# Kernel tuning notes

Hardware: AMD Instinct MI355X
Metric: run time of the kernel (lower is better)

## Reference

```python
import jax, jax.numpy as jnp
import numpy as np

B, S, HID = 4, 1024, 768
H, D = 12, 32              # attention_head_size = (HID/H)//2
AH = H * D                 # all_head_size = 384
SCALING = D ** (-0.5)


def setup_inputs() -> dict:
    key = jax.random.key(0)
    ks = jax.random.split(key, 6)
    hidden_states = jax.random.normal(ks[0], (B, S, HID), dtype=jnp.float32)
    attention_mask = jnp.zeros((B, 1, 1, S), dtype=jnp.float32)
    init = 0.02
    Wq = jax.random.normal(ks[1], (AH, HID), dtype=jnp.float32) * init
    Wk1 = jax.random.normal(ks[2], (AH, HID), dtype=jnp.float32) * init
    Wk2 = jax.random.normal(ks[3], (AH, HID), dtype=jnp.float32) * init
    Wv = jax.random.normal(ks[4], (AH, HID), dtype=jnp.float32) * init
    bq = jnp.zeros((AH,), jnp.float32)
    bk1 = jnp.zeros((AH,), jnp.float32)
    bk2 = jnp.zeros((AH,), jnp.float32)
    bv = jnp.zeros((AH,), jnp.float32)
    pi = jnp.ones((2, H), jnp.float32) / 2.0
    return {"hidden_states": hidden_states, "attention_mask": attention_mask,
            "Wq": Wq, "bq": bq, "Wk1": Wk1, "bk1": bk1, "Wk2": Wk2, "bk2": bk2,
            "Wv": Wv, "bv": bv, "pi": pi}


def _heads(x):
    # [B,S,AH] -> [B,H,S,D]
    return x.reshape(B, S, H, D).transpose(0, 2, 1, 3)


def _sq_dist(x1, x2):
    # gpytorch Distance._sq_dist (postprocess=False): mean-adjust, then
    # ||x1||^2 + ||x2||^2 - 2 x1 x2^T, clamped at 0.
    adj = x1.mean(axis=-2, keepdims=True)
    x1 = x1 - adj
    x2 = x2 - adj
    n1 = (x1 * x1).sum(-1, keepdims=True)            # [B,H,S,1]
    n2 = (x2 * x2).sum(-1, keepdims=True)            # [B,H,S,1]
    cross = jnp.einsum('bhqd,bhkd->bhqk', x1, x2)    # [B,H,S,S]
    return jnp.maximum(n1 + jnp.swapaxes(n2, -1, -2) - 2.0 * cross, 0.0)


def reference(hidden_states, attention_mask, Wq, bq, Wk1, bk1, Wk2, bk2, Wv, bv, pi):
    q = _heads(hidden_states @ Wq.T + bq)
    k1 = _heads(hidden_states @ Wk1.T + bk1)
    k2 = _heads(hidden_states @ Wk2.T + bk2)
    v = _heads(hidden_states @ Wv.T + bv)

    d1 = -SCALING / 2.0 * _sq_dist(q, k1) + attention_mask
    d2 = -1.5 * SCALING / 2.0 * _sq_dist(q, k2) + attention_mask
    d1 = d1 - d1.max(axis=-1, keepdims=True)
    d2 = d2 - d2.max(axis=-1, keepdims=True)

    pi_c = jnp.clip(pi, 1e-6, 2.0)                   # clamp per original
    scores = (jnp.exp(d1) * pi_c[0][None, :, None, None]
              + jnp.exp(d2) * pi_c[1][None, :, None, None])
    probs = scores / (scores.sum(axis=-1, keepdims=True) + 1e-6)
    # dropout is identity in eval mode
    ctx = jnp.einsum('bhqk,bhkd->bhqd', probs, v)
    ctx = ctx.transpose(0, 2, 1, 3).reshape(B, S, AH)
    return (ctx, probs)
```

## Files before the change

### kernel.cpp

```cpp
#include <hip/hip_runtime.h>
#include <math.h>

#define BB 4
#define SS 1024
#define HH 12
#define DD 32
#define HIDDEN 768
#define AHS 384
#define RQ 8
#define HEAD_ELEMS (SS*DD)
#define CTX_ELEMS (BB*SS*AHS)

__device__ __forceinline__ float clampf(float x, float lo, float hi){ return fminf(fmaxf(x, lo), hi); }

__global__ __launch_bounds__(256)
void proj_kernel(const float* __restrict__ X,
                 const float* __restrict__ W0, const float* __restrict__ b0,
                 const float* __restrict__ W1, const float* __restrict__ b1,
                 const float* __restrict__ W2, const float* __restrict__ b2,
                 const float* __restrict__ W3, const float* __restrict__ b3,
                 float* __restrict__ qo, float* __restrict__ k1o,
                 float* __restrict__ k2o, float* __restrict__ vo)
{
    const int BM = 128, BN = 64, BK = 16;
    __shared__ float Xs[BK][BM + 4];
    __shared__ float Wsh[BK][BN + 4];
    int t  = threadIdx.x;
    int m0 = blockIdx.x * BM;
    int n0 = blockIdx.y * BN;
    int mat = n0 / AHS;
    int c0  = n0 % AHS;
    const float* W    = (mat==0) ? W0 : (mat==1) ? W1 : (mat==2) ? W2 : W3;
    const float* bias = (mat==0) ? b0 : (mat==1) ? b1 : (mat==2) ? b2 : b3;

    int tx = t & 15, ty = t >> 4;
    int lr = t >> 2;
    int lc = (t & 3) << 2;

    float acc[8][4];
    #pragma unroll
    for (int i = 0; i < 8; i++)
        #pragma unroll
        for (int j = 0; j < 4; j++) acc[i][j] = 0.f;

    float4 xa = *(const float4*)(X + (m0 + lr) * HIDDEN + lc);
    float4 xb = *(const float4*)(X + (m0 + 64 + lr) * HIDDEN + lc);
    float4 wa = *(const float4*)(W + (c0 + lr) * HIDDEN + lc);

    for (int k0 = 0; k0 < HIDDEN; k0 += BK) {
        __syncthreads();
        Xs[lc+0][lr] = xa.x; Xs[lc+1][lr] = xa.y; Xs[lc+2][lr] = xa.z; Xs[lc+3][lr] = xa.w;
        Xs[lc+0][64+lr] = xb.x; Xs[lc+1][64+lr] = xb.y; Xs[lc+2][64+lr] = xb.z; Xs[lc+3][64+lr] = xb.w;
        Wsh[lc+0][lr] = wa.x; Wsh[lc+1][lr] = wa.y; Wsh[lc+2][lr] = wa.z; Wsh[lc+3][lr] = wa.w;
        __syncthreads();
        if (k0 + BK < HIDDEN) {
            xa = *(const float4*)(X + (m0 + lr) * HIDDEN + k0 + BK + lc);
            xb = *(const float4*)(X + (m0 + 64 + lr) * HIDDEN + k0 + BK + lc);
            wa = *(const float4*)(W + (c0 + lr) * HIDDEN + k0 + BK + lc);
        }
        #pragma unroll
        for (int kk = 0; kk < BK; kk++) {
            float a[8], w4[4];
            *(float4*)&a[0] = *(const float4*)&Xs[kk][ty << 3];
            *(float4*)&a[4] = *(const float4*)&Xs[kk][(ty << 3) + 4];
            *(float4*)w4    = *(const float4*)&Wsh[kk][tx << 2];
            #pragma unroll
            for (int i = 0; i < 8; i++)
                #pragma unroll
                for (int j = 0; j < 4; j++)
                    acc[i][j] = fmaf(a[i], w4[j], acc[i][j]);
        }
    }

    int cbase = c0 + (tx << 2);
    int h  = (cbase >> 5) % HH;
    int d0 = cbase & 31;
    int d4 = d0 >> 2;
    float4 bq4 = *(const float4*)(bias + cbase);

    #pragma unroll
    for (int i = 0; i < 8; i++) {
        int row = m0 + (ty << 3) + i;
        int b_  = row >> 10;
        int s   = row & 1023;
        int bh  = b_ * HH + h;
        float4 val;
        val.x = acc[i][0] + bq4.x;
        val.y = acc[i][1] + bq4.y;
        val.z = acc[i][2] + bq4.z;
        val.w = acc[i][3] + bq4.w;
        if (mat == 0)
            *(float4*)&qo[((size_t)(bh * SS + s)) * DD + d0] = val;
        else if (mat == 1)
            *(float4*)&k1o[((size_t)(bh * 8 + d4) * SS + s) * 4] = val;
        else if (mat == 2)
            *(float4*)&k2o[((size_t)(bh * 8 + d4) * SS + s) * 4] = val;
        else
            *(float4*)&vo[((size_t)(bh * SS + s)) * DD + d0] = val;
    }
}

__global__ __launch_bounds__(256)
void norms_kernel(const float* __restrict__ k1i, const float* __restrict__ k2i,
                  float* __restrict__ n1, float* __restrict__ n2)
{
    int bh = blockIdx.y;
    int s  = blockIdx.x * 256 + threadIdx.x;
    const float* p1 = k1i + (size_t)bh * (8 * SS * 4) + s * 4;
    const float* p2 = k2i + (size_t)bh * (8 * SS * 4) + s * 4;
    float a1 = 0.f, a2 = 0.f;
    #pragma unroll
    for (int d4 = 0; d4 < 8; d4++) {
        float4 v1 = *(const float4*)&p1[(size_t)d4 * SS * 4];
        float4 v2 = *(const float4*)&p2[(size_t)d4 * SS * 4];
        a1 = fmaf(v1.x, v1.x, a1); a1 = fmaf(v1.y, v1.y, a1);
        a1 = fmaf(v1.z, v1.z, a1); a1 = fmaf(v1.w, v1.w, a1);
        a2 = fmaf(v2.x, v2.x, a2); a2 = fmaf(v2.y, v2.y, a2);
        a2 = fmaf(v2.z, v2.z, a2); a2 = fmaf(v2.w, v2.w, a2);
    }
    n1[bh * SS + s] = a1;
    n2[bh * SS + s] = a2;
}

__global__ __launch_bounds__(256, 4)
void attn_fused(const float* __restrict__ qg,  const float* __restrict__ k1i,
                const float* __restrict__ k2i,
                const float* __restrict__ n1g, const float* __restrict__ n2g,
                const float* __restrict__ maskg, const float* __restrict__ pig,
                const float* __restrict__ vg,
                float* __restrict__ probs, float* __restrict__ ctx)
{
    const float A1C = 0.08838834764831845f;
    const float A2C = 0.13258252147247767f;
    __shared__ float p_s[RQ * SS];
    __shared__ float q_s[RQ * DD];
    __shared__ float red1[4][RQ], red2[4][RQ];
    __shared__ float qn_s[RQ];

    int t    = threadIdx.x;
    int lane = t & 63, wid = t >> 6;

    int bid = blockIdx.x;
    int swz = (bid & 7) * 768 + (bid >> 3);
    int bh  = swz >> 7;
    int s0  = (swz & 127) * RQ;
    int b   = bh / HH, h = bh - b * HH;

    q_s[t] = qg[(bh * SS + s0) * DD + t];
    __syncthreads();
    if (t < RQ) {
        float a = 0.f;
        for (int d = 0; d < DD; d++) { float x = q_s[t * DD + d]; a = fmaf(x, x, a); }
        qn_s[t] = a;
    }
    __syncthreads();

    float pi0 = clampf(pig[h],      1e-6f, 2.0f);
    float pi1 = clampf(pig[HH + h], 1e-6f, 2.0f);

    float e1r[4][RQ], e2r[4][RQ];
    float pm1[RQ], pm2[RQ];
    #pragma unroll
    for (int r = 0; r < RQ; r++) { pm1[r] = -3.4e38f; pm2[r] = -3.4e38f; }

    const float* k1p = k1i + (size_t)bh * (8 * SS * 4);
    const float* k2p = k2i + (size_t)bh * (8 * SS * 4);
    const float* n1p = n1g + bh * SS;
    const float* n2p = n2g + bh * SS;
    const float* mp  = maskg + b * SS;

    #pragma unroll
    for (int j = 0; j < 4; j++) {
        int k = j * 256 + t;
        float n1k = n1p[k], n2k = n2p[k], mk = mp[k];
        float c1[RQ], c2[RQ];
        #pragma unroll
        for (int r = 0; r < RQ; r++) { c1[r] = 0.f; c2[r] = 0.f; }
        #pragma unroll
        for (int d4 = 0; d4 < 8; d4++) {
            float4 kq1 = *(const float4*)&k1p[((size_t)d4 * SS + k) * 4];
            float4 kq2 = *(const float4*)&k2p[((size_t)d4 * SS + k) * 4];
            const float* kv1 = (const float*)&kq1;
            const float* kv2 = (const float*)&kq2;
            #pragma unroll
            for (int r = 0; r < RQ; r++) {
                float qv[4];
                *(float4*)qv = *(const float4*)&q_s[r * DD + d4 * 4];
                #pragma unroll
                for (int dd = 0; dd < 4; dd++) {
                    c1[r] = fmaf(qv[dd], kv1[dd], c1[r]);
                    c2[r] = fmaf(qv[dd], kv2[dd], c2[r]);
                }
            }
        }
        #pragma unroll
        for (int r = 0; r < RQ; r++) {
            float qn  = qn_s[r];
            float d1v = fmaxf(fmaf(-2.f, c1[r], qn + n1k), 0.f);
            float d2v = fmaxf(fmaf(-2.f, c2[r], qn + n2k), 0.f);
            float ev1 = fmaf(-A1C, d1v, mk);
            float ev2 = fmaf(-A2C, d2v, mk);
            e1r[j][r] = ev1;
            e2r[j][r] = ev2;
            pm1[r] = fmaxf(pm1[r], ev1);
            pm2[r] = fmaxf(pm2[r], ev2);
        }
    }

    #pragma unroll
    for (int off = 32; off >= 1; off >>= 1)
        #pragma unroll
        for (int r = 0; r < RQ; r++) {
            pm1[r] = fmaxf(pm1[r], __shfl_xor(pm1[r], off));
            pm2[r] = fmaxf(pm2[r], __shfl_xor(pm2[r], off));
        }
    if (lane == 0) {
        #pragma unroll
        for (int r = 0; r < RQ; r++) { red1[wid][r] = pm1[r]; red2[wid][r] = pm2[r]; }
    }
    __syncthreads();
    float m1[RQ], m2[RQ];
    #pragma unroll
    for (int r = 0; r < RQ; r++) {
        m1[r] = fmaxf(fmaxf(red1[0][r], red1[1][r]), fmaxf(red1[2][r], red1[3][r]));
        m2[r] = fmaxf(fmaxf(red2[0][r], red2[1][r]), fmaxf(red2[2][r], red2[3][r]));
    }

    float ps[RQ];
    #pragma unroll
    for (int r = 0; r < RQ; r++) ps[r] = 0.f;
    #pragma unroll
    for (int j = 0; j < 4; j++)
        #pragma unroll
        for (int r = 0; r < RQ; r++) {
            float p = pi0 * __expf(e1r[j][r] - m1[r]) + pi1 * __expf(e2r[j][r] - m2[r]);
            e1r[j][r] = p;
            ps[r] += p;
        }

    #pragma unroll
    for (int off = 32; off >= 1; off >>= 1)
        #pragma unroll
        for (int r = 0; r < RQ; r++) ps[r] += __shfl_xor(ps[r], off);
    __syncthreads();
    if (lane == 0) {
        #pragma unroll
        for (int r = 0; r < RQ; r++) red1[wid][r] = ps[r];
    }
    __syncthreads();
    float inv[RQ];
    #pragma unroll
    for (int r = 0; r < RQ; r++) {
        float sum = red1[0][r] + red1[1][r] + red1[2][r] + red1[3][r];
        inv[r] = 1.0f / (sum + 1e-6f);
    }

    float* prow = probs + (size_t)(bh * SS + s0) * SS;
    #pragma unroll
    for (int j = 0; j < 4; j++) {
        int k = (j << 8) + t;
        float pv8[8];
        #pragma unroll
        for (int r = 0; r < RQ; r++) pv8[r] = e1r[j][r] * inv[r];
        #pragma unroll
        for (int r = 0; r < RQ; r++)
            __builtin_nontemporal_store(pv8[r], &prow[(size_t)r * SS + k]);
        int base = (k << 3) ^ (((k >> 5) & 3) << 3);
        *(float4*)&p_s[base]     = *(float4*)&pv8[0];
        *(float4*)&p_s[base + 4] = *(float4*)&pv8[4];
    }
    __syncthreads();

    {
        int ks = t >> 3;
        int c4 = t & 7;
        int swzc = (ks & 3) << 3;
        const float* vp = vg + bh * HEAD_ELEMS + (c4 << 2);
        float4 acc4[RQ];
        #pragma unroll
        for (int r = 0; r < RQ; r++) acc4[r] = make_float4(0.f, 0.f, 0.f, 0.f);
        #pragma unroll 4
        for (int kk = 0; kk < 32; kk++) {
            int k = (ks << 5) + kk;
            int base = (k << 3) ^ swzc;
            float pr[8];
            *(float4*)&pr[0] = *(const float4*)&p_s[base];
            *(float4*)&pr[4] = *(const float4*)&p_s[base + 4];
            float4 vv = *(const float4*)&vp[k << 5];
            #pragma unroll
            for (int r = 0; r < RQ; r++) {
                acc4[r].x = fmaf(pr[r], vv.x, acc4[r].x);
                acc4[r].y = fmaf(pr[r], vv.y, acc4[r].y);
                acc4[r].z = fmaf(pr[r], vv.z, acc4[r].z);
                acc4[r].w = fmaf(pr[r], vv.w, acc4[r].w);
            }
        }
        __syncthreads();
        #pragma unroll
        for (int r = 0; r < RQ; r++)
            *(float4*)&p_s[((ks << 8) + (r << 5) + (c4 << 2)) ^ ((ks & 3) << 3)] = acc4[r];
    }
    __syncthreads();

    {
        int rr = t >> 5, dd = t & 31;
        float o = 0.f;
        #pragma unroll
        for (int s2 = 0; s2 < 32; s2++)
            o += p_s[((s2 << 8) + (rr << 5) + dd) ^ ((s2 & 3) << 3)];
        __builtin_nontemporal_store(o, &ctx[((size_t)(b * SS + s0 + rr) * HH + h) * DD + dd]);
    }
}

extern "C" void kernel_launch(void* const* d_in, const int* in_sizes, int n_in,
                              void* d_out, int out_size, void* d_ws, size_t ws_size,
                              hipStream_t stream)
{
    const float* hs   = (const float*)d_in[0];
    const float* mask = (const float*)d_in[1];
    const float* Wq   = (const float*)d_in[2];
    const float* bq   = (const float*)d_in[3];
    const float* Wk1  = (const float*)d_in[4];
    const float* bk1  = (const float*)d_in[5];
    const float* Wk2  = (const float*)d_in[6];
    const float* bk2  = (const float*)d_in[7];
    const float* Wv   = (const float*)d_in[8];
    const float* bv   = (const float*)d_in[9];
    const float* pi   = (const float*)d_in[10];

    float* ws   = (float*)d_ws;
    float* q_ws = ws;
    float* v_ws = ws + (size_t)CTX_ELEMS * 1;
    float* k1T  = ws + (size_t)CTX_ELEMS * 2;
    float* k2T  = ws + (size_t)CTX_ELEMS * 3;
    float* n1   = ws + (size_t)CTX_ELEMS * 4;
    float* n2   = n1 + BB * HH * SS;

    float* ctx   = (float*)d_out;
    float* probs = ctx + CTX_ELEMS;

    proj_kernel<<<dim3(32, 24), 256, 0, stream>>>(hs, Wq, bq, Wk1, bk1, Wk2, bk2,
                                                  Wv, bv, q_ws, k1T, k2T, v_ws);
    norms_kernel<<<dim3(SS / 256, BB * HH), 256, 0, stream>>>(k1T, k2T, n1, n2);
    attn_fused<<<dim3(BB * HH * (SS / RQ)), 256, 0, stream>>>(q_ws, k1T, k2T,
                                                              n1, n2, mask, pi,
                                                              v_ws, probs, ctx);
}
```

Baseline: 519.9 us.

## Split attention into two staged score passes, fuse key norms into projection

The attention kernel now computes the k1 and k2 distance scores in two separate passes. The first pass's logits are staged in shared memory instead of being held alongside the second pass in registers, which cuts register pressure; an amdgpu_waves_per_eu(4,4) hint is added. Softmax normalization is deferred, so ctx is scaled by the inverse sum at the end and the probs stores move after the PV product as regular stores. The separate norms kernel is removed: k1/k2 squared norms are reduced inside the projection epilogue, and the projection GEMM gets double-buffered shared memory. The trade-off is extra shared-memory traffic and more barriers in exchange for fewer registers and one fewer launch.

New measurement: 1.332 ms. +156.1%, slower.

```diff
diff --git a/kernel.cpp b/kernel.cpp
--- a/kernel.cpp
+++ b/kernel.cpp
@@ -20,11 +20,12 @@
                  const float* __restrict__ W2, const float* __restrict__ b2,
                  const float* __restrict__ W3, const float* __restrict__ b3,
                  float* __restrict__ qo, float* __restrict__ k1o,
-                 float* __restrict__ k2o, float* __restrict__ vo)
+                 float* __restrict__ k2o, float* __restrict__ vo,
+                 float* __restrict__ n1, float* __restrict__ n2)
 {
     const int BM = 128, BN = 64, BK = 16;
-    __shared__ float Xs[BK][BM + 4];
-    __shared__ float Wsh[BK][BN + 4];
+    __shared__ float Xs[2][BK][BM + 4];
+    __shared__ float Wsh[2][BK][BN + 4];
     int t  = threadIdx.x;
     int m0 = blockIdx.x * BM;
     int n0 = blockIdx.y * BN;
@@ -47,13 +48,15 @@
     float4 xb = *(const float4*)(X + (m0 + 64 + lr) * HIDDEN + lc);
     float4 wa = *(const float4*)(W + (c0 + lr) * HIDDEN + lc);
 
+    Xs[0][lc+0][lr] = xa.x; Xs[0][lc+1][lr] = xa.y; Xs[0][lc+2][lr] = xa.z; Xs[0][lc+3][lr] = xa.w;
+    Xs[0][lc+0][64+lr] = xb.x; Xs[0][lc+1][64+lr] = xb.y; Xs[0][lc+2][64+lr] = xb.z; Xs[0][lc+3][64+lr] = xb.w;
+    Wsh[0][lc+0][lr] = wa.x; Wsh[0][lc+1][lr] = wa.y; Wsh[0][lc+2][lr] = wa.z; Wsh[0][lc+3][lr] = wa.w;
+    __syncthreads();
+
     for (int k0 = 0; k0 < HIDDEN; k0 += BK) {
-        __syncthreads();
-        Xs[lc+0][lr] = xa.x; Xs[lc+1][lr] = xa.y; Xs[lc+2][lr] = xa.z; Xs[lc+3][lr] = xa.w;
-        Xs[lc+0][64+lr] = xb.x; Xs[lc+1][64+lr] = xb.y; Xs[lc+2][64+lr] = xb.z; Xs[lc+3][64+lr] = xb.w;
-        Wsh[lc+0][lr] = wa.x; Wsh[lc+1][lr] = wa.y; Wsh[lc+2][lr] = wa.z; Wsh[lc+3][lr] = wa.w;
-        __syncthreads();
-        if (k0 + BK < HIDDEN) {
+        int cur = (k0 >> 4) & 1;
+        bool more = (k0 + BK < HIDDEN);
+        if (more) {
             xa = *(const float4*)(X + (m0 + lr) * HIDDEN + k0 + BK + lc);
             xb = *(const float4*)(X + (m0 + 64 + lr) * HIDDEN + k0 + BK + lc);
             wa = *(const float4*)(W + (c0 + lr) * HIDDEN + k0 + BK + lc);
@@ -61,23 +64,31 @@
         #pragma unroll
         for (int kk = 0; kk < BK; kk++) {
             float a[8], w4[4];
-            *(float4*)&a[0] = *(const float4*)&Xs[kk][ty << 3];
-            *(float4*)&a[4] = *(const float4*)&Xs[kk][(ty << 3) + 4];
-            *(float4*)w4    = *(const float4*)&Wsh[kk][tx << 2];
+            *(float4*)&a[0] = *(const float4*)&Xs[cur][kk][ty << 3];
+            *(float4*)&a[4] = *(const float4*)&Xs[cur][kk][(ty << 3) + 4];
+            *(float4*)w4    = *(const float4*)&Wsh[cur][kk][tx << 2];
             #pragma unroll
             for (int i = 0; i < 8; i++)
                 #pragma unroll
                 for (int j = 0; j < 4; j++)
                     acc[i][j] = fmaf(a[i], w4[j], acc[i][j]);
         }
+        if (more) {
+            int nxt = cur ^ 1;
+            Xs[nxt][lc+0][lr] = xa.x; Xs[nxt][lc+1][lr] = xa.y; Xs[nxt][lc+2][lr] = xa.z; Xs[nxt][lc+3][lr] = xa.w;
+            Xs[nxt][lc+0][64+lr] = xb.x; Xs[nxt][lc+1][64+lr] = xb.y; Xs[nxt][lc+2][64+lr] = xb.z; Xs[nxt][lc+3][64+lr] = xb.w;
+            Wsh[nxt][lc+0][lr] = wa.x; Wsh[nxt][lc+1][lr] = wa.y; Wsh[nxt][lc+2][lr] = wa.z; Wsh[nxt][lc+3][lr] = wa.w;
+            __syncthreads();
+        }
     }
 
     int cbase = c0 + (tx << 2);
-    int h  = (cbase >> 5) % HH;
+    int h  = cbase >> 5;
     int d0 = cbase & 31;
     int d4 = d0 >> 2;
     float4 bq4 = *(const float4*)(bias + cbase);
 
+    float psq[8];
     #pragma unroll
     for (int i = 0; i < 8; i++) {
         int row = m0 + (ty << 3) + i;
@@ -89,6 +100,7 @@
         val.y = acc[i][1] + bq4.y;
         val.z = acc[i][2] + bq4.z;
         val.w = acc[i][3] + bq4.w;
+        psq[i] = val.x*val.x + val.y*val.y + val.z*val.z + val.w*val.w;
         if (mat == 0)
             *(float4*)&qo[((size_t)(bh * SS + s)) * DD + d0] = val;
         else if (mat == 1)
@@ -98,31 +110,31 @@
         else
             *(float4*)&vo[((size_t)(bh * SS + s)) * DD + d0] = val;
     }
+
+    if (mat == 1 || mat == 2) {
+        float* nout = (mat == 1) ? n1 : n2;
+        float* nrm  = (float*)Xs;
+        __syncthreads();
+        int hs = tx >> 3, q8 = tx & 7;
+        #pragma unroll
+        for (int i = 0; i < 8; i++)
+            nrm[hs * 1024 + ((ty << 3) + i) * 8 + q8] = psq[i];
+        __syncthreads();
+        int hs2 = t >> 7, ri = t & 127;
+        const float* pn = &nrm[hs2 * 1024 + ri * 8];
+        float4 aq = *(const float4*)pn;
+        float4 bq = *(const float4*)(pn + 4);
+        float s8 = ((aq.x + aq.y) + (aq.z + aq.w)) + ((bq.x + bq.y) + (bq.z + bq.w));
+        int row = m0 + ri;
+        int b_  = row >> 10;
+        int s   = row & 1023;
+        int hh  = (c0 >> 5) + hs2;
+        nout[(b_ * HH + hh) * SS + s] = s8;
+    }
 }
 
 __global__ __launch_bounds__(256)
-void norms_kernel(const float* __restrict__ k1i, const float* __restrict__ k2i,
-                  float* __restrict__ n1, float* __restrict__ n2)
-{
-    int bh = blockIdx.y;
-    int s  = blockIdx.x * 256 + threadIdx.x;
-    const float* p1 = k1i + (size_t)bh * (8 * SS * 4) + s * 4;
-    const float* p2 = k2i + (size_t)bh * (8 * SS * 4) + s * 4;
-    float a1 = 0.f, a2 = 0.f;
-    #pragma unroll
-    for (int d4 = 0; d4 < 8; d4++) {
-        float4 v1 = *(const float4*)&p1[(size_t)d4 * SS * 4];
-        float4 v2 = *(const float4*)&p2[(size_t)d4 * SS * 4];
-        a1 = fmaf(v1.x, v1.x, a1); a1 = fmaf(v1.y, v1.y, a1);
-        a1 = fmaf(v1.z, v1.z, a1); a1 = fmaf(v1.w, v1.w, a1);
-        a2 = fmaf(v2.x, v2.x, a2); a2 = fmaf(v2.y, v2.y, a2);
-        a2 = fmaf(v2.z, v2.z, a2); a2 = fmaf(v2.w, v2.w, a2);
-    }
-    n1[bh * SS + s] = a1;
-    n2[bh * SS + s] = a2;
-}
-
-__global__ __launch_bounds__(256, 4)
+__attribute__((amdgpu_waves_per_eu(4, 4)))
 void attn_fused(const float* __restrict__ qg,  const float* __restrict__ k1i,
                 const float* __restrict__ k2i,
                 const float* __restrict__ n1g, const float* __restrict__ n2g,
@@ -158,86 +170,128 @@
     float pi0 = clampf(pig[h],      1e-6f, 2.0f);
     float pi1 = clampf(pig[HH + h], 1e-6f, 2.0f);
 
-    float e1r[4][RQ], e2r[4][RQ];
-    float pm1[RQ], pm2[RQ];
-    #pragma unroll
-    for (int r = 0; r < RQ; r++) { pm1[r] = -3.4e38f; pm2[r] = -3.4e38f; }
-
     const float* k1p = k1i + (size_t)bh * (8 * SS * 4);
     const float* k2p = k2i + (size_t)bh * (8 * SS * 4);
     const float* n1p = n1g + bh * SS;
     const float* n2p = n2g + bh * SS;
     const float* mp  = maskg + b * SS;
 
+    float pm1[RQ];
+    #pragma unroll
+    for (int r = 0; r < RQ; r++) pm1[r] = -3.4e38f;
     #pragma unroll
     for (int j = 0; j < 4; j++) {
-        int k = j * 256 + t;
-        float n1k = n1p[k], n2k = n2p[k], mk = mp[k];
-        float c1[RQ], c2[RQ];
-        #pragma unroll
-        for (int r = 0; r < RQ; r++) { c1[r] = 0.f; c2[r] = 0.f; }
+        int k = (j << 8) + t;
+        float n1k = n1p[k], mk = mp[k];
+        float c1[RQ];
+        #pragma unroll
+        for (int r = 0; r < RQ; r++) c1[r] = 0.f;
         #pragma unroll
         for (int d4 = 0; d4 < 8; d4++) {
             float4 kq1 = *(const float4*)&k1p[((size_t)d4 * SS + k) * 4];
+            const float* kv1 = (const float*)&kq1;
+            #pragma unroll
+            for (int r = 0; r < RQ; r++) {
+                float qv[4];
+                *(float4*)qv = *(const float4*)&q_s[r * DD + d4 * 4];
+                #pragma unroll
+                for (int dd = 0; dd < 4; dd++)
+                    c1[r] = fmaf(qv[dd], kv1[dd], c1[r]);
+            }
+        }
+        float pv8[8];
+        #pragma unroll
+        for (int r = 0; r < RQ; r++) {
+            float d1v = fmaxf(fmaf(-2.f, c1[r], qn_s[r] + n1k), 0.f);
+            float ev1 = fmaf(-A1C, d1v, mk);
+            pv8[r] = ev1;
+            pm1[r] = fmaxf(pm1[r], ev1);
+        }
+        int base = (k << 3) ^ (((k >> 5) & 3) << 3);
+        *(float4*)&p_s[base]     = *(float4*)&pv8[0];
+        *(float4*)&p_s[base + 4] = *(float4*)&pv8[4];
+    }
+    #pragma unroll
+    for (int off = 32; off >= 1; off >>= 1)
+        #pragma unroll
+        for (int r = 0; r < RQ; r++) pm1[r] = fmaxf(pm1[r], __shfl_xor(pm1[r], off));
+    if (lane == 0) {
+        #pragma unroll
+        for (int r = 0; r < RQ; r++) red1[wid][r] = pm1[r];
+    }
+    __syncthreads();
+    float m1[RQ];
+    #pragma unroll
+    for (int r = 0; r < RQ; r++)
+        m1[r] = fmaxf(fmaxf(red1[0][r], red1[1][r]), fmaxf(red1[2][r], red1[3][r]));
+
+    float e2r[4][RQ];
+    float pm2[RQ];
+    #pragma unroll
+    for (int r = 0; r < RQ; r++) pm2[r] = -3.4e38f;
+    #pragma unroll
+    for (int j = 0; j < 4; j++) {
+        int k = (j << 8) + t;
+        float n2k = n2p[k], mk = mp[k];
+        float c2[RQ];
+        #pragma unroll
+        for (int r = 0; r < RQ; r++) c2[r] = 0.f;
+        #pragma unroll
+        for (int d4 = 0; d4 < 8; d4++) {
             float4 kq2 = *(const float4*)&k2p[((size_t)d4 * SS + k) * 4];
-            const float* kv1 = (const float*)&kq1;
             const float* kv2 = (const float*)&kq2;
             #pragma unroll
             for (int r = 0; r < RQ; r++) {
                 float qv[4];
                 *(float4*)qv = *(const float4*)&q_s[r * DD + d4 * 4];
                 #pragma unroll
-                for (int dd = 0; dd < 4; dd++) {
-                    c1[r] = fmaf(qv[dd], kv1[dd], c1[r]);
+                for (int dd = 0; dd < 4; dd++)
                     c2[r] = fmaf(qv[dd], kv2[dd], c2[r]);
-                }
             }
         }
         #pragma unroll
         for (int r = 0; r < RQ; r++) {
-            float qn  = qn_s[r];
-            float d1v = fmaxf(fmaf(-2.f, c1[r], qn + n1k), 0.f);
-            float d2v = fmaxf(fmaf(-2.f, c2[r], qn + n2k), 0.f);
-            float ev1 = fmaf(-A1C, d1v, mk);
+            float d2v = fmaxf(fmaf(-2.f, c2[r], qn_s[r] + n2k), 0.f);
             float ev2 = fmaf(-A2C, d2v, mk);
-            e1r[j][r] = ev1;
             e2r[j][r] = ev2;
-            pm1[r] = fmaxf(pm1[r], ev1);
             pm2[r] = fmaxf(pm2[r], ev2);
         }
     }
-
     #pragma unroll
     for (int off = 32; off >= 1; off >>= 1)
         #pragma unroll
+        for (int r = 0; r < RQ; r++) pm2[r] = fmaxf(pm2[r], __shfl_xor(pm2[r], off));
+    if (lane == 0) {
+        #pragma unroll
+        for (int r = 0; r < RQ; r++) red2[wid][r] = pm2[r];
+    }
+    __syncthreads();
+    float m2[RQ];
+    #pragma unroll
+    for (int r = 0; r < RQ; r++)
+        m2[r] = fmaxf(fmaxf(red2[0][r], red2[1][r]), fmaxf(red2[2][r], red2[3][r]));
+
+    float ps[RQ];
+    #pragma unroll
+    for (int r = 0; r < RQ; r++) ps[r] = 0.f;
+    #pragma unroll
+    for (int j = 0; j < 4; j++) {
+        int k = (j << 8) + t;
+        int base = (k << 3) ^ (((k >> 5) & 3) << 3);
+        float ev1[8];
+        *(float4*)&ev1[0] = *(const float4*)&p_s[base];
+        *(float4*)&ev1[4] = *(const float4*)&p_s[base + 4];
+        float pv8[8];
+        #pragma unroll
         for (int r = 0; r < RQ; r++) {
-            pm1[r] = fmaxf(pm1[r], __shfl_xor(pm1[r], off));
-            pm2[r] = fmaxf(pm2[r], __shfl_xor(pm2[r], off));
-        }
-    if (lane == 0) {
-        #pragma unroll
-        for (int r = 0; r < RQ; r++) { red1[wid][r] = pm1[r]; red2[wid][r] = pm2[r]; }
-    }
-    __syncthreads();
-    float m1[RQ], m2[RQ];
-    #pragma unroll
-    for (int r = 0; r < RQ; r++) {
-        m1[r] = fmaxf(fmaxf(red1[0][r], red1[1][r]), fmaxf(red1[2][r], red1[3][r]));
-        m2[r] = fmaxf(fmaxf(red2[0][r], red2[1][r]), fmaxf(red2[2][r], red2[3][r]));
-    }
-
-    float ps[RQ];
-    #pragma unroll
-    for (int r = 0; r < RQ; r++) ps[r] = 0.f;
-    #pragma unroll
-    for (int j = 0; j < 4; j++)
-        #pragma unroll
-        for (int r = 0; r < RQ; r++) {
-            float p = pi0 * __expf(e1r[j][r] - m1[r]) + pi1 * __expf(e2r[j][r] - m2[r]);
-            e1r[j][r] = p;
+            float p = pi0 * __expf(ev1[r] - m1[r]) + pi1 * __expf(e2r[j][r] - m2[r]);
+            e2r[j][r] = p;
+            pv8[r] = p;
             ps[r] += p;
         }
-
+        *(float4*)&p_s[base]     = *(float4*)&pv8[0];
+        *(float4*)&p_s[base + 4] = *(float4*)&pv8[4];
+    }
     #pragma unroll
     for (int off = 32; off >= 1; off >>= 1)
         #pragma unroll
@@ -254,22 +308,6 @@
         float sum = red1[0][r] + red1[1][r] + red1[2][r] + red1[3][r];
         inv[r] = 1.0f / (sum + 1e-6f);
     }
-
-    float* prow = probs + (size_t)(bh * SS + s0) * SS;
-    #pragma unroll
-    for (int j = 0; j < 4; j++) {
-        int k = (j << 8) + t;
-        float pv8[8];
-        #pragma unroll
-        for (int r = 0; r < RQ; r++) pv8[r] = e1r[j][r] * inv[r];
-        #pragma unroll
-        for (int r = 0; r < RQ; r++)
-            __builtin_nontemporal_store(pv8[r], &prow[(size_t)r * SS + k]);
-        int base = (k << 3) ^ (((k >> 5) & 3) << 3);
-        *(float4*)&p_s[base]     = *(float4*)&pv8[0];
-        *(float4*)&p_s[base + 4] = *(float4*)&pv8[4];
-    }
-    __syncthreads();
 
     {
         int ks = t >> 3;
@@ -308,7 +346,18 @@
         #pragma unroll
         for (int s2 = 0; s2 < 32; s2++)
             o += p_s[((s2 << 8) + (rr << 5) + dd) ^ ((s2 & 3) << 3)];
-        __builtin_nontemporal_store(o, &ctx[((size_t)(b * SS + s0 + rr) * HH + h) * DD + dd]);
+        float sum = red1[0][rr] + red1[1][rr] + red1[2][rr] + red1[3][rr];
+        o *= 1.0f / (sum + 1e-6f);
+        ctx[((size_t)(b * SS + s0 + rr) * HH + h) * DD + dd] = o;
+    }
+
+    float* prow = probs + (size_t)(bh * SS + s0) * SS;
+    #pragma unroll
+    for (int j = 0; j < 4; j++) {
+        int k = (j << 8) + t;
+        #pragma unroll
+        for (int r = 0; r < RQ; r++)
+            prow[(size_t)r * SS + k] = e2r[j][r] * inv[r];
     }
 }
 
@@ -340,8 +389,8 @@
     float* probs = ctx + CTX_ELEMS;
 
     proj_kernel<<<dim3(32, 24), 256, 0, stream>>>(hs, Wq, bq, Wk1, bk1, Wk2, bk2,
-                                                  Wv, bv, q_ws, k1T, k2T, v_ws);
-    norms_kernel<<<dim3(SS / 256, BB * HH), 256, 0, stream>>>(k1T, k2T, n1, n2);
+                                                  Wv, bv, q_ws, k1T, k2T, v_ws,
+                                                  n1, n2);
     attn_fused<<<dim3(BB * HH * (SS / RQ)), 256, 0, stream>>>(q_ws, k1T, k2T,
                                                               n1, n2, mask, pi,
                                                               v_ws, probs, ctx);
```
